# Kernel optimization log

Measured on AMD Instinct MI355X. Metric: run time of the kernel, lower is better.

Reference implementation:

```python
import jax, jax.numpy as jnp
import numpy as np

N, T, C = 100000, 12, 32  # nodes, periods, hidden (A3TGCN out_channels hardcoded 32)
E = 3_200_000


def setup_inputs() -> dict:
    key = jax.random.key(0)
    ks = jax.random.split(key, 20)
    s_g = 1.0 / np.sqrt(1.0)        # GCNConv glorot-ish for in=1
    s_l = 1.0 / np.sqrt(2.0 * C)    # torch Linear default for in=2C
    s_h = 1.0 / np.sqrt(C)
    u = lambda k, shape, s: jax.random.uniform(k, shape, jnp.float32, -s, s)
    return {
        "x": jax.random.normal(ks[0], (N, T), jnp.float32),
        "edge_index": jax.random.randint(ks[1], (2, E), 0, N, jnp.int32),
        "edge_weight": jax.random.uniform(ks[2], (E,), jnp.float32),
        # TGCN gate GCNConv params (in_channels=1, out=C)
        "w_z": u(ks[3], (1, C), s_g), "b_z": jnp.zeros((C,), jnp.float32),
        "w_r": u(ks[4], (1, C), s_g), "b_r": jnp.zeros((C,), jnp.float32),
        "w_h": u(ks[5], (1, C), s_g), "b_h": jnp.zeros((C,), jnp.float32),
        # TGCN gate Linear params (torch layout [out=C, in=2C])
        "lw_z": u(ks[6], (C, 2 * C), s_l), "lb_z": u(ks[7], (C,), s_l),
        "lw_r": u(ks[8], (C, 2 * C), s_l), "lb_r": u(ks[9], (C,), s_l),
        "lw_h": u(ks[10], (C, 2 * C), s_l), "lb_h": u(ks[11], (C,), s_l),
        # A3TGCN temporal attention
        "att": jax.random.uniform(ks[12], (T,), jnp.float32),
        # head Linear(32, 1)
        "head_w": u(ks[13], (1, C), s_h), "head_b": u(ks[14], (1,), s_h),
    }


def reference(x, edge_index, edge_weight, w_z, b_z, w_r, b_r, w_h, b_h,
              lw_z, lb_z, lw_r, lb_r, lw_h, lb_h, att, head_w, head_b):
    n = x.shape[0]
    # --- GCN normalization with self-loops (fill value 1) ---
    loop = jnp.arange(n)
    s = jnp.concatenate([edge_index[0], loop])
    d = jnp.concatenate([edge_index[1], loop])
    w = jnp.concatenate([edge_weight, jnp.ones((n,), edge_weight.dtype)])
    deg = jax.ops.segment_sum(w, d, num_segments=n)
    dinv = jnp.where(deg > 0, jax.lax.rsqrt(deg), 0.0)
    norm = dinv[s] * w * dinv[d]
    # --- shared sparse aggregation: A_hat @ X for all periods at once ---
    # in_channels = 1, so GCNConv(X_t) = (A_hat x_t) * W + b; aggregate scalars [N,T]
    agg = jax.ops.segment_sum(norm[:, None] * x[s], d, num_segments=n)  # [N, T]
    # gate convolutions, [N, T, C]
    cz = agg[:, :, None] * w_z[0] + b_z
    ch = agg[:, :, None] * w_h[0] + b_h
    # A3TGCN passes H=None every period -> hidden starts at 0 each step, so
    # linear([conv, H]) reduces to conv @ W[:, :C].T + b, and the reset gate R
    # multiplies H=0 (no effect on output).
    Z = jax.nn.sigmoid(jnp.einsum('ntc,oc->nto', cz, lw_z[:, :C]) + lb_z)
    Ht = jnp.tanh(jnp.einsum('ntc,oc->nto', ch, lw_h[:, :C]) + lb_h)
    Hp = (1.0 - Z) * Ht  # per-period hidden state, [N, T, C]
    probs = jax.nn.softmax(att)
    h = jnp.einsum('t,ntc->nc', probs, Hp)  # attention-weighted temporal sum
    h = jax.nn.relu(h)
    return h @ head_w.T + head_b  # [N, 1]
```

## Files before the change

### kernel.cpp

```cpp
#include <hip/hip_runtime.h>
#include <hip/hip_fp16.h>

#define N_NODES 100000
#define T_P 12
#define C_H 32
#define E_EDGES 3200000

#define NODES_PER_B 256
#define NB 391
#define CAPA 8704

#define VEC_E (E_EDGES / 4)
#define P1_THREADS 512
#define P1_VECS 2048
#define NBLK1 ((VEC_E + P1_VECS - 1) / P1_VECS)


__global__ void __launch_bounds__(512)
bucket_scatter_kernel(const int* __restrict__ src, const int* __restrict__ dst,
                      const float* __restrict__ w, int* __restrict__ cursor,
                      float2* __restrict__ entries) {
    __shared__ int h[NB];
    __shared__ int claim[NB];
    int tid = threadIdx.x;
    int vbase = blockIdx.x * P1_VECS;
    for (int i = tid; i < NB; i += 512) h[i] = 0;
    __syncthreads();
    const int4* d4 = (const int4*)dst;
    int4 dc[4];
    int rra[16];
#pragma unroll
    for (int q = 0; q < 4; ++q) {
        int v = vbase + q * 512 + tid;
        if (v < VEC_E) {
            int4 d = d4[v];
            dc[q] = d;
            rra[q * 4 + 0] = atomicAdd(&h[d.x >> 8], 1);
            rra[q * 4 + 1] = atomicAdd(&h[d.y >> 8], 1);
            rra[q * 4 + 2] = atomicAdd(&h[d.z >> 8], 1);
            rra[q * 4 + 3] = atomicAdd(&h[d.w >> 8], 1);
        }
    }
    __syncthreads();
    for (int i = tid; i < NB; i += 512) {
        int c = h[i];
        claim[i] = c ? atomicAdd(&cursor[i], c) : 0;
    }
    __syncthreads();
    const int4* s4 = (const int4*)src;
    const float4* w4 = (const float4*)w;
#pragma unroll
    for (int q = 0; q < 4; ++q) {
        int v = vbase + q * 512 + tid;
        if (v < VEC_E) {
            int4 d = dc[q];
            int4 s = s4[v];
            float4 ww = w4[v];
            int bin, dl, pos;
            bin = d.x >> 8; dl = d.x & 255; pos = claim[bin] + rra[q * 4 + 0];
            if (pos < CAPA) entries[(size_t)bin * CAPA + pos] = make_float2(__int_as_float(s.x | (dl << 17)), ww.x);
            bin = d.y >> 8; dl = d.y & 255; pos = claim[bin] + rra[q * 4 + 1];
            if (pos < CAPA) entries[(size_t)bin * CAPA + pos] = make_float2(__int_as_float(s.y | (dl << 17)), ww.y);
            bin = d.z >> 8; dl = d.z & 255; pos = claim[bin] + rra[q * 4 + 2];
            if (pos < CAPA) entries[(size_t)bin * CAPA + pos] = make_float2(__int_as_float(s.z | (dl << 17)), ww.z);
            bin = d.w >> 8; dl = d.w & 255; pos = claim[bin] + rra[q * 4 + 3];
            if (pos < CAPA) entries[(size_t)bin * CAPA + pos] = make_float2(__int_as_float(s.w | (dl << 17)), ww.w);
        }
    }
}

__global__ void __launch_bounds__(1024)
prep_kernel(const float2* __restrict__ entries, const int* __restrict__ cursor,
            const float* __restrict__ x, float* __restrict__ dinv, __half* __restrict__ y,
            const float* __restrict__ wz, const float* __restrict__ bz,
            const float* __restrict__ wh, const float* __restrict__ bh,
            const float* __restrict__ lwz, const float* __restrict__ lbz,
            const float* __restrict__ lwh, const float* __restrict__ lbh,
            const float* __restrict__ att, float* __restrict__ P) {
    __shared__ float wsum[NODES_PER_B];
    __shared__ float dloc[NODES_PER_B];
    int tid = threadIdx.x;
    int b = blockIdx.x;
    int nbase = b << 8;
    size_t lo = (size_t)b * CAPA;
    int ne = cursor[b]; if (ne > CAPA) ne = CAPA;
    if (tid < NODES_PER_B) wsum[tid] = 0.f;
    __syncthreads();
    for (int k = tid; k < ne; k += 1024) {
        float2 e = entries[lo + k];
        atomicAdd(&wsum[(__float_as_int(e.x) >> 17) & 255], e.y);
    }
    __syncthreads();
    if (tid < NODES_PER_B) {
        int n = nbase + tid;
        float di = (n < N_NODES) ? rsqrtf(1.0f + wsum[tid]) : 0.f;
        dloc[tid] = di;
        if (n < N_NODES) dinv[n] = di;
    }
    __syncthreads();
    if (tid < 512) {
        int nl = tid >> 1, q = tid & 1;
        int n = nbase + nl;
        if (n < N_NODES) {
            float di = dloc[nl];
            union { __half h[8]; float4 f4; } u;
            if (q == 0) {
                float4 a = ((const float4*)x)[(size_t)n * 3 + 0];
                float4 c = ((const float4*)x)[(size_t)n * 3 + 1];
                u.h[0] = __float2half_rn(a.x * di); u.h[1] = __float2half_rn(a.y * di);
                u.h[2] = __float2half_rn(a.z * di); u.h[3] = __float2half_rn(a.w * di);
                u.h[4] = __float2half_rn(c.x * di); u.h[5] = __float2half_rn(c.y * di);
                u.h[6] = __float2half_rn(c.z * di); u.h[7] = __float2half_rn(c.w * di);
            } else {
                float4 c = ((const float4*)x)[(size_t)n * 3 + 2];
                u.h[0] = __float2half_rn(c.x * di); u.h[1] = __float2half_rn(c.y * di);
                u.h[2] = __float2half_rn(c.z * di); u.h[3] = __float2half_rn(c.w * di);
                u.h[4] = __ushort_as_half((unsigned short)0);
                u.h[5] = __ushort_as_half((unsigned short)0);
                u.h[6] = __ushort_as_half((unsigned short)0);
                u.h[7] = __ushort_as_half((unsigned short)0);
            }
            ((float4*)y)[((size_t)n << 1) + q] = u.f4;
        }
    }
    if (b == 0) {
        int o = tid;
        if (o < C_H) {
            float az = 0.f, bzv = 0.f, ah = 0.f, bhv = 0.f;
            for (int c = 0; c < C_H; ++c) {
                float lz = lwz[o * 2 * C_H + c];
                float lh = lwh[o * 2 * C_H + c];
                az += wz[c] * lz;  bzv += bz[c] * lz;
                ah += wh[c] * lh;  bhv += bh[c] * lh;
            }
            P[16 + o]  = az;  P[48 + o]  = bzv + lbz[o];
            P[80 + o]  = ah;  P[112 + o] = bhv + lbh[o];
        }
        if (o == 0) {
            float m = -1e30f;
            for (int t = 0; t < T_P; ++t) m = fmaxf(m, att[t]);
            float e[T_P], s = 0.f;
            for (int t = 0; t < T_P; ++t) { e[t] = __expf(att[t] - m); s += e[t]; }
            float inv = 1.0f / s;
            for (int t = 0; t < T_P; ++t) P[t] = e[t] * inv;
        }
    }
}

__global__ void __launch_bounds__(1024, 8)
sort_gather_kernel(const float2* __restrict__ entries, const int* __restrict__ cursor,
                   const float* __restrict__ dinv, const __half* __restrict__ y,
                   const float* __restrict__ P, const float* __restrict__ head_w,
                   const float* __restrict__ head_b, float* __restrict__ out) {
    __shared__ float2 stage[CAPA];
    __shared__ int   cnt[NODES_PER_B];
    __shared__ int   inc[NODES_PER_B];
    __shared__ float Ps[160];
    __shared__ float hws[C_H];
    int tid = threadIdx.x;
    int b = blockIdx.x;
    size_t lo = (size_t)b * CAPA;
    int ne = cursor[b]; if (ne > CAPA) ne = CAPA;
    if (tid < 160) Ps[tid] = P[tid];
    if (tid < C_H) hws[tid] = head_w[tid];
    if (tid < NODES_PER_B) cnt[tid] = 0;
    __syncthreads();
    float2 ent[9];
    int    rr[9];
#pragma unroll
    for (int i = 0; i < 9; ++i) {
        int k = tid + i * 1024;
        if (k < ne) {
            float2 e = entries[lo + k];
            ent[i] = e;
            rr[i] = atomicAdd(&cnt[(__float_as_int(e.x) >> 17) & 255], 1);
        }
    }
    __syncthreads();
    if (tid < NODES_PER_B) inc[tid] = cnt[tid];
    __syncthreads();
    for (int d = 1; d < NODES_PER_B; d <<= 1) {
        int t = (tid >= d && tid < NODES_PER_B) ? inc[tid - d] : 0;
        __syncthreads();
        if (tid < NODES_PER_B) inc[tid] += t;
        __syncthreads();
    }
#pragma unroll
    for (int i = 0; i < 9; ++i) {
        int k = tid + i * 1024;
        if (k < ne) {
            int dl = (__float_as_int(ent[i].x) >> 17) & 255;
            stage[inc[dl] - cnt[dl] + rr[i]] = ent[i];
        }
    }
    __syncthreads();
    int nl = tid >> 2, lane = tid & 3;
    int n = (b << 8) + nl;
    if (n >= N_NODES) return;
    int end = inc[nl];
    int start = end - cnt[nl];
    float4 a0 = make_float4(0.f, 0.f, 0.f, 0.f);
    float4 a1 = a0, a2 = a0;
    if (lane == 0) {
        const float4* yn = (const float4*)(y + ((size_t)n << 4));
        float4 r0 = yn[0], r1 = yn[1];
        const __half2* hp = (const __half2*)&r0;
        const __half2* hq = (const __half2*)&r1;
        float2 p0 = __half22float2(hp[0]), p1 = __half22float2(hp[1]);
        float2 p2 = __half22float2(hp[2]), p3 = __half22float2(hp[3]);
        float2 p4 = __half22float2(hq[0]), p5 = __half22float2(hq[1]);
        a0 = make_float4(p0.x, p0.y, p1.x, p1.y);
        a1 = make_float4(p2.x, p2.y, p3.x, p3.y);
        a2 = make_float4(p4.x, p4.y, p5.x, p5.y);
    }
    for (int j = start + lane; j < end; j += 4) {
        float2 e = stage[j];
        int s = __float_as_int(e.x) & 0x1FFFF;
        float c = e.y;
        const float4* ys = (const float4*)(y + ((size_t)s << 4));
        float4 r0 = ys[0], r1 = ys[1];
        const __half2* hp = (const __half2*)&r0;
        const __half2* hq = (const __half2*)&r1;
        float2 p0 = __half22float2(hp[0]), p1 = __half22float2(hp[1]);
        float2 p2 = __half22float2(hp[2]), p3 = __half22float2(hp[3]);
        float2 p4 = __half22float2(hq[0]), p5 = __half22float2(hq[1]);
        a0.x += c * p0.x; a0.y += c * p0.y; a0.z += c * p1.x; a0.w += c * p1.y;
        a1.x += c * p2.x; a1.y += c * p2.y; a1.z += c * p3.x; a1.w += c * p3.y;
        a2.x += c * p4.x; a2.y += c * p4.y; a2.z += c * p5.x; a2.w += c * p5.y;
    }
#define RED4(v) v += __shfl_xor(v, 1); v += __shfl_xor(v, 2)
    RED4(a0.x); RED4(a0.y); RED4(a0.z); RED4(a0.w);
    RED4(a1.x); RED4(a1.y); RED4(a1.z); RED4(a1.w);
    RED4(a2.x); RED4(a2.y); RED4(a2.z); RED4(a2.w);
#undef RED4
    float din = dinv[n];
    float av[T_P];
    av[0] = a0.x * din; av[1] = a0.y * din; av[2]  = a0.z * din; av[3]  = a0.w * din;
    av[4] = a1.x * din; av[5] = a1.y * din; av[6]  = a1.z * din; av[7]  = a1.w * din;
    av[8] = a2.x * din; av[9] = a2.y * din; av[10] = a2.z * din; av[11] = a2.w * din;
    float acc = 0.f;
#pragma unroll
    for (int k = 0; k < 8; ++k) {
        int c = (lane << 3) + k;
        float Az = Ps[16 + c], Bz = Ps[48 + c], Ah = Ps[80 + c], Bh = Ps[112 + c];
        float hc = 0.f;
#pragma unroll
        for (int t = 0; t < T_P; ++t) {
            float a = av[t];
            float oz = 1.f / (1.f + __expf(a * Az + Bz));
            float vv = a * Ah + Bh;
            float th = 1.f - 2.f / (1.f + __expf(2.f * vv));
            hc += Ps[t] * oz * th;
        }
        acc += fmaxf(hc, 0.f) * hws[c];
    }
    acc += __shfl_xor(acc, 1);
    acc += __shfl_xor(acc, 2);
    if (lane == 0) out[n] = acc + head_b[0];
}

extern "C" void kernel_launch(void* const* d_in, const int* in_sizes, int n_in,
                              void* d_out, int out_size, void* d_ws, size_t ws_size,
                              hipStream_t stream) {
    const float* x    = (const float*)d_in[0];
    const int*   ei   = (const int*)d_in[1];
    const float* ew   = (const float*)d_in[2];
    const float* w_z  = (const float*)d_in[3];
    const float* b_z  = (const float*)d_in[4];
    const float* w_h  = (const float*)d_in[7];
    const float* b_h  = (const float*)d_in[8];
    const float* lw_z = (const float*)d_in[9];
    const float* lb_z = (const float*)d_in[10];
    const float* lw_h = (const float*)d_in[13];
    const float* lb_h = (const float*)d_in[14];
    const float* att  = (const float*)d_in[15];
    const float* hw   = (const float*)d_in[16];
    const float* hb   = (const float*)d_in[17];
    float* out = (float*)d_out;

    float* wsf      = (float*)d_ws;
    float* P        = wsf;
    float* dinv     = P + 256;
    int*   cursor   = (int*)(dinv + N_NODES);
    __half* y       = (__half*)(wsf + 100656);
    float2* entries = (float2*)(wsf + 100656 + (size_t)N_NODES * 8);

    const int* srcp = ei;
    const int* dstp = ei + E_EDGES;

    hipMemsetAsync(cursor, 0, NB * sizeof(int), stream);
    bucket_scatter_kernel<<<NBLK1, P1_THREADS, 0, stream>>>(srcp, dstp, ew, cursor, entries);
    prep_kernel<<<NB, 1024, 0, stream>>>(entries, cursor, x, dinv, y,
                                         w_z, b_z, w_h, b_h, lw_z, lb_z, lw_h, lb_h, att, P);
    sort_gather_kernel<<<NB, 1024, 0, stream>>>(entries, cursor, dinv, y, P, hw, hb, out);
}
```

Baseline: 237.4 us.

## Split each bucket across two blocks and pack staged edges into 32 bits

The final gather kernel now launches two 512-thread blocks per 256-node bucket, each handling one half of the destination nodes. Both blocks read the whole bucket's entries twice and keep only their half. Staged records are packed into one 32-bit word (17-bit source plus an fp16 edge weight), which cuts shared memory per block and is meant to allow more resident blocks and parallelism. The cost is double global reads of the entries, fp16 rounding of the normalized weights, and silent truncation if a half-bucket exceeds the stage capacity.

```diff
diff --git a/kernel.cpp b/kernel.cpp
--- a/kernel.cpp
+++ b/kernel.cpp
@@ -9,6 +9,8 @@
 #define NODES_PER_B 256
 #define NB 391
 #define CAPA 8704
+#define NFINE 782
+#define HSTAGE 4608
 
 #define VEC_E (E_EDGES / 4)
 #define P1_THREADS 512
@@ -147,58 +149,66 @@
     }
 }
 
-__global__ void __launch_bounds__(1024, 8)
+__global__ void __launch_bounds__(512, 8)
 sort_gather_kernel(const float2* __restrict__ entries, const int* __restrict__ cursor,
                    const float* __restrict__ dinv, const __half* __restrict__ y,
                    const float* __restrict__ P, const float* __restrict__ head_w,
                    const float* __restrict__ head_b, float* __restrict__ out) {
-    __shared__ float2 stage[CAPA];
-    __shared__ int   cnt[NODES_PER_B];
-    __shared__ int   inc[NODES_PER_B];
+    __shared__ unsigned int stage[HSTAGE];
+    __shared__ int   cnt[128];
+    __shared__ int   inc[128];
     __shared__ float Ps[160];
     __shared__ float hws[C_H];
     int tid = threadIdx.x;
-    int b = blockIdx.x;
-    size_t lo = (size_t)b * CAPA;
-    int ne = cursor[b]; if (ne > CAPA) ne = CAPA;
+    int f = blockIdx.x;
+    int c = f >> 1;
+    int hsel = (f & 1) << 7;
+    size_t lo = (size_t)c * CAPA;
+    int ne = cursor[c]; if (ne > CAPA) ne = CAPA;
     if (tid < 160) Ps[tid] = P[tid];
     if (tid < C_H) hws[tid] = head_w[tid];
-    if (tid < NODES_PER_B) cnt[tid] = 0;
-    __syncthreads();
-    float2 ent[9];
-    int    rr[9];
-#pragma unroll
-    for (int i = 0; i < 9; ++i) {
-        int k = tid + i * 1024;
+    if (tid < 128) cnt[tid] = 0;
+    __syncthreads();
+    int rra[17];
+#pragma unroll
+    for (int i = 0; i < 17; ++i) {
+        int k = tid + i * 512;
+        if (k < ne) {
+            int u = __float_as_int(entries[lo + k].x);
+            int dl = (u >> 17) & 255;
+            if ((dl & 128) == hsel) rra[i] = atomicAdd(&cnt[dl & 127], 1);
+        }
+    }
+    __syncthreads();
+    if (tid < 128) inc[tid] = cnt[tid];
+    __syncthreads();
+    for (int d = 1; d < 128; d <<= 1) {
+        int t = (tid >= d && tid < 128) ? inc[tid - d] : 0;
+        __syncthreads();
+        if (tid < 128) inc[tid] += t;
+        __syncthreads();
+    }
+#pragma unroll
+    for (int i = 0; i < 17; ++i) {
+        int k = tid + i * 512;
         if (k < ne) {
             float2 e = entries[lo + k];
-            ent[i] = e;
-            rr[i] = atomicAdd(&cnt[(__float_as_int(e.x) >> 17) & 255], 1);
-        }
-    }
-    __syncthreads();
-    if (tid < NODES_PER_B) inc[tid] = cnt[tid];
-    __syncthreads();
-    for (int d = 1; d < NODES_PER_B; d <<= 1) {
-        int t = (tid >= d && tid < NODES_PER_B) ? inc[tid - d] : 0;
-        __syncthreads();
-        if (tid < NODES_PER_B) inc[tid] += t;
-        __syncthreads();
-    }
-#pragma unroll
-    for (int i = 0; i < 9; ++i) {
-        int k = tid + i * 1024;
-        if (k < ne) {
-            int dl = (__float_as_int(ent[i].x) >> 17) & 255;
-            stage[inc[dl] - cnt[dl] + rr[i]] = ent[i];
+            int u = __float_as_int(e.x);
+            int dl = (u >> 17) & 255;
+            if ((dl & 128) == hsel) {
+                int dlf = dl & 127;
+                int pos = inc[dlf] - cnt[dlf] + rra[i];
+                unsigned int hb = (unsigned int)__half_as_ushort(__float2half_rn(e.y));
+                if (pos < HSTAGE) stage[pos] = (unsigned int)(u & 0x1FFFF) | (hb << 17);
+            }
         }
     }
     __syncthreads();
     int nl = tid >> 2, lane = tid & 3;
-    int n = (b << 8) + nl;
+    int n = (f << 7) + nl;
     if (n >= N_NODES) return;
-    int end = inc[nl];
-    int start = end - cnt[nl];
+    int end = inc[nl]; if (end > HSTAGE) end = HSTAGE;
+    int start = end - cnt[nl]; if (start < 0) start = 0;
     float4 a0 = make_float4(0.f, 0.f, 0.f, 0.f);
     float4 a1 = a0, a2 = a0;
     if (lane == 0) {
@@ -214,9 +224,9 @@
         a2 = make_float4(p4.x, p4.y, p5.x, p5.y);
     }
     for (int j = start + lane; j < end; j += 4) {
-        float2 e = stage[j];
-        int s = __float_as_int(e.x) & 0x1FFFF;
-        float c = e.y;
+        unsigned int rec = stage[j];
+        int s = rec & 0x1FFFF;
+        float cw = __half2float(__ushort_as_half((unsigned short)(rec >> 17)));
         const float4* ys = (const float4*)(y + ((size_t)s << 4));
         float4 r0 = ys[0], r1 = ys[1];
         const __half2* hp = (const __half2*)&r0;
@@ -224,9 +234,9 @@
         float2 p0 = __half22float2(hp[0]), p1 = __half22float2(hp[1]);
         float2 p2 = __half22float2(hp[2]), p3 = __half22float2(hp[3]);
         float2 p4 = __half22float2(hq[0]), p5 = __half22float2(hq[1]);
-        a0.x += c * p0.x; a0.y += c * p0.y; a0.z += c * p1.x; a0.w += c * p1.y;
-        a1.x += c * p2.x; a1.y += c * p2.y; a1.z += c * p3.x; a1.w += c * p3.y;
-        a2.x += c * p4.x; a2.y += c * p4.y; a2.z += c * p5.x; a2.w += c * p5.y;
+        a0.x += cw * p0.x; a0.y += cw * p0.y; a0.z += cw * p1.x; a0.w += cw * p1.y;
+        a1.x += cw * p2.x; a1.y += cw * p2.y; a1.z += cw * p3.x; a1.w += cw * p3.y;
+        a2.x += cw * p4.x; a2.y += cw * p4.y; a2.z += cw * p5.x; a2.w += cw * p5.y;
     }
 #define RED4(v) v += __shfl_xor(v, 1); v += __shfl_xor(v, 2)
     RED4(a0.x); RED4(a0.y); RED4(a0.z); RED4(a0.w);
@@ -241,8 +251,8 @@
     float acc = 0.f;
 #pragma unroll
     for (int k = 0; k < 8; ++k) {
-        int c = (lane << 3) + k;
-        float Az = Ps[16 + c], Bz = Ps[48 + c], Ah = Ps[80 + c], Bh = Ps[112 + c];
+        int ch = (lane << 3) + k;
+        float Az = Ps[16 + ch], Bz = Ps[48 + ch], Ah = Ps[80 + ch], Bh = Ps[112 + ch];
         float hc = 0.f;
 #pragma unroll
         for (int t = 0; t < T_P; ++t) {
@@ -252,7 +262,7 @@
             float th = 1.f - 2.f / (1.f + __expf(2.f * vv));
             hc += Ps[t] * oz * th;
         }
-        acc += fmaxf(hc, 0.f) * hws[c];
+        acc += fmaxf(hc, 0.f) * hws[ch];
     }
     acc += __shfl_xor(acc, 1);
     acc += __shfl_xor(acc, 2);
@@ -292,5 +302,5 @@
     bucket_scatter_kernel<<<NBLK1, P1_THREADS, 0, stream>>>(srcp, dstp, ew, cursor, entries);
     prep_kernel<<<NB, 1024, 0, stream>>>(entries, cursor, x, dinv, y,
                                          w_z, b_z, w_h, b_h, lw_z, lb_z, lw_h, lb_h, att, P);
-    sort_gather_kernel<<<NB, 1024, 0, stream>>>(entries, cursor, dinv, y, P, hw, hb, out);
+    sort_gather_kernel<<<NFINE, 512, 0, stream>>>(entries, cursor, dinv, y, P, hw, hb, out);
 }
```

New measurement: 252.8 us. 1.06x slower.

## Replace global-atomic bucket scatter with per-window local sort and count table

Applied to the files above, without the earlier changes.

The first pass now writes each window's edges into its own contiguous region, sorted by destination bucket through a block-local exclusive scan. It records per-window bucket offsets in a count table, which removes the global cursor atomics and the memset. The consumer kernels rebuild each bucket's entries by scanning the 391 window lengths and doing a binary search per entry. The scatter writes become more coalesced and contention-free, at the cost of extra scans, binary searches and fragmented reads in prep and gather. It also drops the CAPA overflow guard on writes, relying on the window size bound.

```diff
diff --git a/kernel.cpp b/kernel.cpp
--- a/kernel.cpp
+++ b/kernel.cpp
@@ -9,21 +9,23 @@
 #define NODES_PER_B 256
 #define NB 391
 #define CAPA 8704
+#define NW 391
+#define WEDGE 8192
 
 #define VEC_E (E_EDGES / 4)
-#define P1_THREADS 512
 #define P1_VECS 2048
-#define NBLK1 ((VEC_E + P1_VECS - 1) / P1_VECS)
 
 
 __global__ void __launch_bounds__(512)
-bucket_scatter_kernel(const int* __restrict__ src, const int* __restrict__ dst,
-                      const float* __restrict__ w, int* __restrict__ cursor,
+window_scatter_kernel(const int* __restrict__ src, const int* __restrict__ dst,
+                      const float* __restrict__ w, int* __restrict__ cnt_tab,
                       float2* __restrict__ entries) {
     __shared__ int h[NB];
-    __shared__ int claim[NB];
+    __shared__ int buf[512];
+    __shared__ int excl[NB];
     int tid = threadIdx.x;
-    int vbase = blockIdx.x * P1_VECS;
+    int wdw = blockIdx.x;
+    int vbase = wdw * P1_VECS;
     for (int i = tid; i < NB; i += 512) h[i] = 0;
     __syncthreads();
     const int4* d4 = (const int4*)dst;
@@ -42,13 +44,24 @@
         }
     }
     __syncthreads();
-    for (int i = tid; i < NB; i += 512) {
-        int c = h[i];
-        claim[i] = c ? atomicAdd(&cursor[i], c) : 0;
-    }
+    buf[tid] = (tid < NB) ? h[tid] : 0;
+    __syncthreads();
+    for (int d_ = 1; d_ < 512; d_ <<= 1) {
+        int t = (tid >= d_) ? buf[tid - d_] : 0;
+        __syncthreads();
+        buf[tid] += t;
+        __syncthreads();
+    }
+    if (tid < NB) {
+        int ex = buf[tid] - h[tid];
+        excl[tid] = ex;
+        cnt_tab[wdw * 392 + tid] = ex;
+    }
+    if (tid == 0) cnt_tab[wdw * 392 + NB] = buf[511];
     __syncthreads();
     const int4* s4 = (const int4*)src;
     const float4* w4 = (const float4*)w;
+    size_t wb = (size_t)wdw * WEDGE;
 #pragma unroll
     for (int q = 0; q < 4; ++q) {
         int v = vbase + q * 512 + tid;
@@ -56,38 +69,58 @@
             int4 d = dc[q];
             int4 s = s4[v];
             float4 ww = w4[v];
-            int bin, dl, pos;
-            bin = d.x >> 8; dl = d.x & 255; pos = claim[bin] + rra[q * 4 + 0];
-            if (pos < CAPA) entries[(size_t)bin * CAPA + pos] = make_float2(__int_as_float(s.x | (dl << 17)), ww.x);
-            bin = d.y >> 8; dl = d.y & 255; pos = claim[bin] + rra[q * 4 + 1];
-            if (pos < CAPA) entries[(size_t)bin * CAPA + pos] = make_float2(__int_as_float(s.y | (dl << 17)), ww.y);
-            bin = d.z >> 8; dl = d.z & 255; pos = claim[bin] + rra[q * 4 + 2];
-            if (pos < CAPA) entries[(size_t)bin * CAPA + pos] = make_float2(__int_as_float(s.z | (dl << 17)), ww.z);
-            bin = d.w >> 8; dl = d.w & 255; pos = claim[bin] + rra[q * 4 + 3];
-            if (pos < CAPA) entries[(size_t)bin * CAPA + pos] = make_float2(__int_as_float(s.w | (dl << 17)), ww.w);
+            int bin, dl;
+            bin = d.x >> 8; dl = d.x & 255;
+            entries[wb + excl[bin] + rra[q * 4 + 0]] = make_float2(__int_as_float(s.x | (dl << 17)), ww.x);
+            bin = d.y >> 8; dl = d.y & 255;
+            entries[wb + excl[bin] + rra[q * 4 + 1]] = make_float2(__int_as_float(s.y | (dl << 17)), ww.y);
+            bin = d.z >> 8; dl = d.z & 255;
+            entries[wb + excl[bin] + rra[q * 4 + 2]] = make_float2(__int_as_float(s.z | (dl << 17)), ww.z);
+            bin = d.w >> 8; dl = d.w & 255;
+            entries[wb + excl[bin] + rra[q * 4 + 3]] = make_float2(__int_as_float(s.w | (dl << 17)), ww.w);
         }
     }
 }
 
 __global__ void __launch_bounds__(1024)
-prep_kernel(const float2* __restrict__ entries, const int* __restrict__ cursor,
+prep_kernel(const float2* __restrict__ entries, const int* __restrict__ cnt_tab,
             const float* __restrict__ x, float* __restrict__ dinv, __half* __restrict__ y,
             const float* __restrict__ wz, const float* __restrict__ bz,
             const float* __restrict__ wh, const float* __restrict__ bh,
             const float* __restrict__ lwz, const float* __restrict__ lbz,
             const float* __restrict__ lwh, const float* __restrict__ lbh,
             const float* __restrict__ att, float* __restrict__ P) {
+    __shared__ int ws_[NW];
+    __shared__ int wo_[NW + 1];
+    __shared__ int sc[1024];
     __shared__ float wsum[NODES_PER_B];
     __shared__ float dloc[NODES_PER_B];
     int tid = threadIdx.x;
     int b = blockIdx.x;
     int nbase = b << 8;
-    size_t lo = (size_t)b * CAPA;
-    int ne = cursor[b]; if (ne > CAPA) ne = CAPA;
+    int len = 0;
+    if (tid < NW) {
+        int s0 = cnt_tab[tid * 392 + b];
+        len = cnt_tab[tid * 392 + b + 1] - s0;
+        ws_[tid] = s0;
+    }
+    sc[tid] = (tid < NW) ? len : 0;
     if (tid < NODES_PER_B) wsum[tid] = 0.f;
     __syncthreads();
-    for (int k = tid; k < ne; k += 1024) {
-        float2 e = entries[lo + k];
+    for (int d_ = 1; d_ < 1024; d_ <<= 1) {
+        int t = (tid >= d_) ? sc[tid - d_] : 0;
+        __syncthreads();
+        sc[tid] += t;
+        __syncthreads();
+    }
+    if (tid < NW) wo_[tid] = sc[tid] - len;
+    if (tid == NW - 1) wo_[NW] = sc[tid];
+    __syncthreads();
+    int ne = wo_[NW]; if (ne > CAPA) ne = CAPA;
+    for (int v = tid; v < ne; v += 1024) {
+        int lo_ = 0, hi_ = NW;
+        while (hi_ - lo_ > 1) { int mid = (lo_ + hi_) >> 1; if (wo_[mid] <= v) lo_ = mid; else hi_ = mid; }
+        float2 e = entries[(size_t)lo_ * WEDGE + ws_[lo_] + (v - wo_[lo_])];
         atomicAdd(&wsum[(__float_as_int(e.x) >> 17) & 255], e.y);
     }
     __syncthreads();
@@ -148,30 +181,50 @@
 }
 
 __global__ void __launch_bounds__(1024, 8)
-sort_gather_kernel(const float2* __restrict__ entries, const int* __restrict__ cursor,
+sort_gather_kernel(const float2* __restrict__ entries, const int* __restrict__ cnt_tab,
                    const float* __restrict__ dinv, const __half* __restrict__ y,
                    const float* __restrict__ P, const float* __restrict__ head_w,
                    const float* __restrict__ head_b, float* __restrict__ out) {
     __shared__ float2 stage[CAPA];
+    __shared__ int   ws_[NW];
+    __shared__ int   wo_[NW + 1];
     __shared__ int   cnt[NODES_PER_B];
     __shared__ int   inc[NODES_PER_B];
     __shared__ float Ps[160];
     __shared__ float hws[C_H];
+    int* sc = (int*)stage;
     int tid = threadIdx.x;
     int b = blockIdx.x;
-    size_t lo = (size_t)b * CAPA;
-    int ne = cursor[b]; if (ne > CAPA) ne = CAPA;
     if (tid < 160) Ps[tid] = P[tid];
     if (tid < C_H) hws[tid] = head_w[tid];
     if (tid < NODES_PER_B) cnt[tid] = 0;
-    __syncthreads();
+    int len = 0;
+    if (tid < NW) {
+        int s0 = cnt_tab[tid * 392 + b];
+        len = cnt_tab[tid * 392 + b + 1] - s0;
+        ws_[tid] = s0;
+    }
+    sc[tid] = (tid < NW) ? len : 0;
+    __syncthreads();
+    for (int d_ = 1; d_ < 1024; d_ <<= 1) {
+        int t = (tid >= d_) ? sc[tid - d_] : 0;
+        __syncthreads();
+        sc[tid] += t;
+        __syncthreads();
+    }
+    if (tid < NW) wo_[tid] = sc[tid] - len;
+    if (tid == NW - 1) wo_[NW] = sc[tid];
+    __syncthreads();
+    int ne = wo_[NW]; if (ne > CAPA) ne = CAPA;
     float2 ent[9];
     int    rr[9];
 #pragma unroll
     for (int i = 0; i < 9; ++i) {
-        int k = tid + i * 1024;
-        if (k < ne) {
-            float2 e = entries[lo + k];
+        int v = tid + i * 1024;
+        if (v < ne) {
+            int lo_ = 0, hi_ = NW;
+            while (hi_ - lo_ > 1) { int mid = (lo_ + hi_) >> 1; if (wo_[mid] <= v) lo_ = mid; else hi_ = mid; }
+            float2 e = entries[(size_t)lo_ * WEDGE + ws_[lo_] + (v - wo_[lo_])];
             ent[i] = e;
             rr[i] = atomicAdd(&cnt[(__float_as_int(e.x) >> 17) & 255], 1);
         }
@@ -179,16 +232,16 @@
     __syncthreads();
     if (tid < NODES_PER_B) inc[tid] = cnt[tid];
     __syncthreads();
-    for (int d = 1; d < NODES_PER_B; d <<= 1) {
-        int t = (tid >= d && tid < NODES_PER_B) ? inc[tid - d] : 0;
+    for (int d_ = 1; d_ < NODES_PER_B; d_ <<= 1) {
+        int t = (tid >= d_ && tid < NODES_PER_B) ? inc[tid - d_] : 0;
         __syncthreads();
         if (tid < NODES_PER_B) inc[tid] += t;
         __syncthreads();
     }
 #pragma unroll
     for (int i = 0; i < 9; ++i) {
-        int k = tid + i * 1024;
-        if (k < ne) {
+        int v = tid + i * 1024;
+        if (v < ne) {
             int dl = (__float_as_int(ent[i].x) >> 17) & 255;
             stage[inc[dl] - cnt[dl] + rr[i]] = ent[i];
         }
@@ -281,16 +334,15 @@
     float* wsf      = (float*)d_ws;
     float* P        = wsf;
     float* dinv     = P + 256;
-    int*   cursor   = (int*)(dinv + N_NODES);
-    __half* y       = (__half*)(wsf + 100656);
-    float2* entries = (float2*)(wsf + 100656 + (size_t)N_NODES * 8);
+    int*   cnt_tab  = (int*)(dinv + N_NODES);
+    __half* y       = (__half*)(wsf + 253536);
+    float2* entries = (float2*)(wsf + 253536 + (size_t)N_NODES * 8);
 
     const int* srcp = ei;
     const int* dstp = ei + E_EDGES;
 
-    hipMemsetAsync(cursor, 0, NB * sizeof(int), stream);
-    bucket_scatter_kernel<<<NBLK1, P1_THREADS, 0, stream>>>(srcp, dstp, ew, cursor, entries);
-    prep_kernel<<<NB, 1024, 0, stream>>>(entries, cursor, x, dinv, y,
+    window_scatter_kernel<<<NW, 512, 0, stream>>>(srcp, dstp, ew, cnt_tab, entries);
+    prep_kernel<<<NB, 1024, 0, stream>>>(entries, cnt_tab, x, dinv, y,
                                          w_z, b_z, w_h, b_h, lw_z, lb_z, lw_h, lb_h, att, P);
-    sort_gather_kernel<<<NB, 1024, 0, stream>>>(entries, cursor, dinv, y, P, hw, hb, out);
+    sort_gather_kernel<<<NB, 1024, 0, stream>>>(entries, cnt_tab, dinv, y, P, hw, hb, out);
 }
```

After: 249.1 us. 1.05x slower.
